# Optimization experiments

Hardware: AMD Instinct MI355X
Metric: run time of the kernel (lower is better)

The kernel has to match this reference:

```python
import jax, jax.numpy as jnp
import numpy as np

N_HEAD = 16
HEAD_DIM = 64
N_EMBD = N_HEAD * HEAD_DIM  # 1024
B, T = 2, 2048


def _rope(x, cos, sin):
    # x: [B,T,H,D]; cos/sin: [1,T,1,D//2]
    d = x.shape[-1] // 2
    x1, x2 = x[..., :d], x[..., d:]
    y1 = x1 * cos + x2 * sin
    y2 = -x1 * sin + x2 * cos
    return jnp.concatenate([y1, y2], axis=-1).astype(x.dtype)


def _rms_norm(x):
    eps = jnp.finfo(x.dtype).eps
    ms = jnp.mean(jnp.square(x), axis=-1, keepdims=True)
    return x * jax.lax.rsqrt(ms + eps)


def setup_inputs() -> dict:
    key = jax.random.key(0)
    ks = jax.random.split(key, 7)
    s = 1.0 / np.sqrt(N_EMBD)
    return {
        "x": jax.random.normal(ks[0], (B, T, N_EMBD), dtype=jnp.float32),
        "cos": jax.random.uniform(ks[1], (1, T, 1, HEAD_DIM // 2), dtype=jnp.float32),
        "sin": jax.random.uniform(ks[2], (1, T, 1, HEAD_DIM // 2), dtype=jnp.float32),
        "Wq": jax.random.normal(ks[3], (N_EMBD, N_EMBD), dtype=jnp.float32) * s,
        "Wk": jax.random.normal(ks[4], (N_EMBD, N_EMBD), dtype=jnp.float32) * s,
        "Wv": jax.random.normal(ks[5], (N_EMBD, N_EMBD), dtype=jnp.float32) * s,
        "Wo": jax.random.normal(ks[6], (N_EMBD, N_EMBD), dtype=jnp.float32) * s,
    }


def reference(x, cos, sin, Wq, Wk, Wv, Wo):
    Bx, Tx, C = x.shape
    # bias-free linear projections (nn.Linear applies x @ W.T)
    q = (x @ Wq.T).reshape(Bx, Tx, N_HEAD, HEAD_DIM)
    k = (x @ Wk.T).reshape(Bx, Tx, N_HEAD, HEAD_DIM)
    v = (x @ Wv.T).reshape(Bx, Tx, N_HEAD, HEAD_DIM)
    # rotary embedding (T == cos length branch)
    q = _rope(q, cos, sin)
    k = _rope(k, cos, sin)
    # QK RMSNorm (no learned scale)
    q = _rms_norm(q)
    k = _rms_norm(k)
    # non-causal SDPA, scale = 1/sqrt(head_dim)
    scale = 1.0 / np.sqrt(HEAD_DIM)
    scores = jnp.einsum("bthd,bshd->bhts", q, k) * scale
    p = jax.nn.softmax(scores, axis=-1)
    y = jnp.einsum("bhts,bshd->bthd", p, v)
    y = y.reshape(Bx, Tx, C)
    return y @ Wo.T
```

## Files before the change

kernel.cpp:

```cpp
#include <hip/hip_runtime.h>
#include <stdint.h>

typedef __attribute__((ext_vector_type(8))) short short8;
typedef __attribute__((ext_vector_type(4))) float floatx4;

#define B_SZ 2
#define T_SZ 2048
#define NH   16
#define HD   64
#define C_SZ 1024
#define M_SZ (B_SZ * T_SZ)

static __device__ __forceinline__ unsigned int cvt2(float a, float b) {
    unsigned int r;
    asm("v_cvt_pk_bf16_f32 %0, %1, %2" : "=v"(r) : "v"(a), "v"(b));
    return r;
}
static __device__ __forceinline__ unsigned short f2bf(float a) {
    return (unsigned short)(cvt2(a, 0.0f) & 0xffffu);
}

static __device__ __forceinline__ void gload_lds16(const void* g, void* l) {
    __builtin_amdgcn_global_load_lds(
        (const __attribute__((address_space(1))) void*)g,
        (__attribute__((address_space(3))) void*)l, 16, 0, 0);
}

__global__ __launch_bounds__(256)
void cvtk(const float* __restrict__ x,
          const float* __restrict__ w0, const float* __restrict__ w1,
          const float* __restrict__ w2, const float* __restrict__ w3,
          unsigned short* __restrict__ xb, unsigned short* __restrict__ wb)
{
    const float* src; unsigned short* dst; int n4;
    const int y = blockIdx.y;
    if (y == 0) { src = x; dst = xb; n4 = (M_SZ * C_SZ) / 4; }
    else {
        src = (y == 1 ? w0 : y == 2 ? w1 : y == 3 ? w2 : w3);
        dst = wb + (size_t)(y - 1) * C_SZ * C_SZ;
        n4 = (C_SZ * C_SZ) / 4;
    }
    for (int i = blockIdx.x * 256 + threadIdx.x; i < n4; i += gridDim.x * 256) {
        float4 f = *(const float4*)&src[(size_t)i * 4];
        uint2 u;
        u.x = cvt2(f.x, f.y);
        u.y = cvt2(f.z, f.w);
        *(uint2*)&dst[(size_t)i * 4] = u;
    }
}

template <int MODE>
__global__ __launch_bounds__(256)
void gemm_nt(const unsigned short* __restrict__ A,
             const unsigned short* __restrict__ Wb,
             const float* __restrict__ cosp,
             const float* __restrict__ sinp,
             unsigned short* __restrict__ qh,
             unsigned short* __restrict__ kh,
             unsigned short* __restrict__ vt,
             float* __restrict__ Cf)
{
    constexpr int K = C_SZ;
    __shared__ __align__(16) unsigned short As[128 * 32];
    __shared__ __align__(16) unsigned short Bs[128 * 32];

    const int tid  = threadIdx.x;
    const int wave = tid >> 6, lane = tid & 63;
    const int wm = wave >> 1, wn = wave & 1;
    const int quad = lane >> 4, l16 = lane & 15;
    const int mb = blockIdx.x * 128, nb = blockIdx.y * 128;
    const int z  = blockIdx.z;

    const unsigned short* Wp = (MODE == 0) ? (Wb + (size_t)z * C_SZ * C_SZ) : Wb;

    floatx4 acc[4][4] = {};

    const int lrow = lane >> 2;
    const int lsw  = lane & 3;

    for (int k0 = 0; k0 < K; k0 += 32) {
        __syncthreads();
        #pragma unroll
        for (int c = 0; c < 2; ++c) {
            int r = (wave * 2 + c) * 16 + lrow;
            int col = ((lsw ^ ((r >> 1) & 3))) * 8;
            gload_lds16(&A[(size_t)(mb + r) * K + k0 + col], &As[(wave * 2 + c) * 512]);
            gload_lds16(&Wp[(size_t)(nb + r) * K + k0 + col], &Bs[(wave * 2 + c) * 512]);
        }
        __syncthreads();

        short8 af[4], bfr[4];
        #pragma unroll
        for (int mt = 0; mt < 4; ++mt) {
            int r = wm * 64 + mt * 16 + l16;
            af[mt] = *(const short8*)&As[r * 32 + ((quad ^ ((r >> 1) & 3)) * 8)];
        }
        #pragma unroll
        for (int nt = 0; nt < 4; ++nt) {
            int r = wn * 64 + nt * 16 + l16;
            bfr[nt] = *(const short8*)&Bs[r * 32 + ((quad ^ ((r >> 1) & 3)) * 8)];
        }
        #pragma unroll
        for (int mt = 0; mt < 4; ++mt)
            #pragma unroll
            for (int nt = 0; nt < 4; ++nt)
                acc[mt][nt] = __builtin_amdgcn_mfma_f32_16x16x32_bf16(
                    af[mt], bfr[nt], acc[mt][nt], 0, 0, 0);
    }

    if (MODE == 1) {
        #pragma unroll
        for (int mt = 0; mt < 4; ++mt)
            #pragma unroll
            for (int nt = 0; nt < 4; ++nt)
                #pragma unroll
                for (int i = 0; i < 4; ++i) {
                    int row = mb + wm * 64 + mt * 16 + quad * 4 + i;
                    int col = nb + wn * 64 + nt * 16 + l16;
                    Cf[(size_t)row * C_SZ + col] = acc[mt][nt][i];
                }
        return;
    }

    const int h = blockIdx.y * 2 + wn;

    if (z == 2) {
        #pragma unroll
        for (int mt = 0; mt < 4; ++mt) {
            int gr0 = mb + wm * 64 + mt * 16 + quad * 4;
            int b = gr0 >> 11, t0 = gr0 & (T_SZ - 1);
            #pragma unroll
            for (int nt = 0; nt < 4; ++nt) {
                int d = nt * 16 + l16;
                uint2 pk;
                pk.x = cvt2(acc[mt][nt][0], acc[mt][nt][1]);
                pk.y = cvt2(acc[mt][nt][2], acc[mt][nt][3]);
                *(uint2*)&vt[((size_t)(b * NH + h) * HD + d) * T_SZ + t0] = pk;
            }
        }
        return;
    }

    unsigned short* dst = (z == 0) ? qh : kh;
    const float qscale = (z == 0) ? (0.125f * 1.4426950408889634f) : 1.0f;
    const float eps = 1.1920929e-07f;

    #pragma unroll
    for (int mt = 0; mt < 4; ++mt) {
        #pragma unroll
        for (int i = 0; i < 4; ++i) {
            int gr = mb + wm * 64 + mt * 16 + quad * 4 + i;
            int b = gr >> 11, t = gr & (T_SZ - 1);
            float ce = cosp[t * 32 + l16];
            float se = sinp[t * 32 + l16];
            float co = cosp[t * 32 + 16 + l16];
            float so = sinp[t * 32 + 16 + l16];
            float a0 = acc[mt][0][i], a1 = acc[mt][1][i];
            float a2 = acc[mt][2][i], a3 = acc[mt][3][i];
            float y0 = a0 * ce + a2 * se;
            float y1 = a1 * co + a3 * so;
            float y2 = a2 * ce - a0 * se;
            float y3 = a3 * co - a1 * so;
            float ss = y0 * y0 + y1 * y1 + y2 * y2 + y3 * y3;
            ss += __shfl_xor(ss, 1, 64);
            ss += __shfl_xor(ss, 2, 64);
            ss += __shfl_xor(ss, 4, 64);
            ss += __shfl_xor(ss, 8, 64);
            float rn = rsqrtf(ss * (1.0f / 64.0f) + eps) * qscale;
            size_t base = ((size_t)(b * NH + h) * T_SZ + t) * (size_t)HD;
            dst[base +  0 + l16] = f2bf(y0 * rn);
            dst[base + 16 + l16] = f2bf(y1 * rn);
            dst[base + 32 + l16] = f2bf(y2 * rn);
            dst[base + 48 + l16] = f2bf(y3 * rn);
        }
    }
}

__global__ __launch_bounds__(512, 4)
void attn(const unsigned short* __restrict__ qh,
          const unsigned short* __restrict__ kh,
          const unsigned short* __restrict__ vt,
          unsigned short* __restrict__ yb)
{
    __shared__ __align__(16) char smem[36864];
    __shared__ float lred[2][128];

    unsigned short* Ks = (unsigned short*)smem;
    unsigned short* Vs = Ks + 64 * 72;
    unsigned short* Psall = Vs + 64 * 72;
    float* Ored = (float*)smem;

    const int tid = threadIdx.x;
    const int wave = tid >> 6, lane = tid & 63;
    const int wk = wave & 1, wq = wave >> 1;
    const int quad = lane >> 4, l16 = lane & 15;
    const int qb = blockIdx.x * 128;
    const int h = blockIdx.y, b = blockIdx.z;

    unsigned short* Ps = Psall + wave * (32 * 36);

    const unsigned short* Qg = qh + ((size_t)(b * NH + h) * T_SZ + qb) * HD;
    const unsigned short* Kg = kh + (size_t)(b * NH + h) * T_SZ * HD;
    const unsigned short* Vg = vt + (size_t)(b * NH + h) * HD * T_SZ;

    short8 qfr[2][2];
    #pragma unroll
    for (int n = 0; n < 2; ++n)
        #pragma unroll
        for (int c = 0; c < 2; ++c)
            qfr[n][c] = *(const short8*)&Qg[(size_t)(wq * 32 + n * 16 + l16) * HD + c * 32 + quad * 8];

    floatx4 o[4][2] = {};
    float l_acc[2] = {0.f, 0.f};

    const int srow = tid >> 3;
    const int scol = (tid & 7) * 8;

    for (int st = 0; st < T_SZ; st += 64) {
        short8 kv = *(const short8*)&Kg[(size_t)(st + srow) * HD + scol];
        short8 vv = *(const short8*)&Vg[(size_t)srow * T_SZ + st + scol];
        *(short8*)&Ks[srow * 72 + scol] = kv;
        *(short8*)&Vs[srow * 72 + scol] = vv;
        __syncthreads();

        floatx4 s[2][2];
        #pragma unroll
        for (int kt = 0; kt < 2; ++kt) {
            const int kr = (wk * 32 + kt * 16 + l16) * 72;
            short8 af0 = *(const short8*)&Ks[kr + quad * 8];
            short8 af1 = *(const short8*)&Ks[kr + 32 + quad * 8];
            #pragma unroll
            for (int n = 0; n < 2; ++n) {
                floatx4 zz = {0.f, 0.f, 0.f, 0.f};
                zz = __builtin_amdgcn_mfma_f32_16x16x32_bf16(af0, qfr[n][0], zz, 0, 0, 0);
                s[kt][n] = __builtin_amdgcn_mfma_f32_16x16x32_bf16(af1, qfr[n][1], zz, 0, 0, 0);
            }
        }

        #pragma unroll
        for (int kt = 0; kt < 2; ++kt)
            #pragma unroll
            for (int n = 0; n < 2; ++n) {
                float p0 = exp2f(s[kt][n][0]);
                float p1 = exp2f(s[kt][n][1]);
                float p2 = exp2f(s[kt][n][2]);
                float p3 = exp2f(s[kt][n][3]);
                l_acc[n] += (p0 + p1) + (p2 + p3);
                uint2 pk;
                pk.x = cvt2(p0, p1);
                pk.y = cvt2(p2, p3);
                *(uint2*)&Ps[(n * 16 + l16) * 36 + kt * 16 + quad * 4] = pk;
            }

        short8 av[4];
        #pragma unroll
        for (int nd = 0; nd < 4; ++nd)
            av[nd] = *(const short8*)&Vs[(nd * 16 + l16) * 72 + wk * 32 + quad * 8];
        #pragma unroll
        for (int nv = 0; nv < 2; ++nv) {
            union { short8 v; uint2 d[2]; } pf;
            pf.d[0] = *(const uint2*)&Ps[(nv * 16 + l16) * 36 + quad * 8];
            pf.d[1] = *(const uint2*)&Ps[(nv * 16 + l16) * 36 + quad * 8 + 4];
            #pragma unroll
            for (int nd = 0; nd < 4; ++nd)
                o[nd][nv] = __builtin_amdgcn_mfma_f32_16x16x32_bf16(av[nd], pf.v, o[nd][nv], 0, 0, 0);
        }
        __syncthreads();
    }

    #pragma unroll
    for (int n = 0; n < 2; ++n) {
        l_acc[n] += __shfl_xor(l_acc[n], 16, 64);
        l_acc[n] += __shfl_xor(l_acc[n], 32, 64);
    }
    if (quad == 0) {
        #pragma unroll
        for (int n = 0; n < 2; ++n)
            lred[wk][wq * 32 + n * 16 + l16] = l_acc[n];
    }
    if (wk == 1) {
        #pragma unroll
        for (int nv = 0; nv < 2; ++nv)
            #pragma unroll
            for (int nd = 0; nd < 4; ++nd)
                *(floatx4*)&Ored[(size_t)wq * (32 * 68) + (nv * 16 + l16) * 68 + nd * 16 + quad * 4] = o[nd][nv];
    }
    __syncthreads();

    if (wk == 0) {
        #pragma unroll
        for (int nv = 0; nv < 2; ++nv) {
            int qi = wq * 32 + nv * 16 + l16;
            float lt = lred[0][qi] + lred[1][qi];
            float inv = 1.0f / lt;
            int t = qb + qi;
            #pragma unroll
            for (int nd = 0; nd < 4; ++nd) {
                floatx4 r = *(const floatx4*)&Ored[(size_t)wq * (32 * 68) + (nv * 16 + l16) * 68 + nd * 16 + quad * 4];
                floatx4 ov = o[nd][nv];
                uint2 u;
                u.x = cvt2((ov[0] + r[0]) * inv, (ov[1] + r[1]) * inv);
                u.y = cvt2((ov[2] + r[2]) * inv, (ov[3] + r[3]) * inv);
                *(uint2*)&yb[((size_t)b * T_SZ + t) * C_SZ + h * 64 + nd * 16 + quad * 4] = u;
            }
        }
    }
}

extern "C" void kernel_launch(void* const* d_in, const int* in_sizes, int n_in,
                              void* d_out, int out_size, void* d_ws, size_t ws_size,
                              hipStream_t stream)
{
    const float* x    = (const float*)d_in[0];
    const float* cosp = (const float*)d_in[1];
    const float* sinp = (const float*)d_in[2];
    const float* Wq   = (const float*)d_in[3];
    const float* Wk   = (const float*)d_in[4];
    const float* Wv   = (const float*)d_in[5];
    const float* Wo   = (const float*)d_in[6];
    float* out = (float*)d_out;

    char* ws = (char*)d_ws;
    unsigned short* xb = (unsigned short*)(ws);
    unsigned short* yb = xb;
    unsigned short* wb = (unsigned short*)(ws + (8u  << 20));
    unsigned short* qh = (unsigned short*)(ws + (16u << 20));
    unsigned short* kh = (unsigned short*)(ws + (24u << 20));
    unsigned short* vt = (unsigned short*)(ws + (32u << 20));

    cvtk<<<dim3(512, 5), 256, 0, stream>>>(x, Wq, Wk, Wv, Wo, xb, wb);
    gemm_nt<0><<<dim3(32, 8, 3), 256, 0, stream>>>(
        xb, wb, cosp, sinp, qh, kh, vt, nullptr);
    attn<<<dim3(16, NH, B_SZ), 512, 0, stream>>>(qh, kh, vt, yb);
    gemm_nt<1><<<dim3(32, 8, 1), 256, 0, stream>>>(
        yb, wb + (size_t)3 * C_SZ * C_SZ, nullptr, nullptr,
        nullptr, nullptr, nullptr, out);
}
```

Measured before the change: 216.3 us.

## Load attention K/V fragments directly from global and double GEMM k-tile

The attention kernel no longer stages K and V tiles through shared memory. Each wave reads its MFMA operand fragments directly from global memory, which removes both block-wide barriers per key tile. The projection GEMM moves to a 64-wide k-step with an 8-way XOR swizzle, halving the loop iterations and barrier count. The cost is redundant global/L2 traffic for K/V across waves and more LDS per GEMM block.

```diff
diff --git a/kernel.cpp b/kernel.cpp
--- a/kernel.cpp
+++ b/kernel.cpp
@@ -61,8 +61,8 @@
              float* __restrict__ Cf)
 {
     constexpr int K = C_SZ;
-    __shared__ __align__(16) unsigned short As[128 * 32];
-    __shared__ __align__(16) unsigned short Bs[128 * 32];
+    __shared__ __align__(16) unsigned short As[128 * 64];
+    __shared__ __align__(16) unsigned short Bs[128 * 64];
 
     const int tid  = threadIdx.x;
     const int wave = tid >> 6, lane = tid & 63;
@@ -75,37 +75,41 @@
 
     floatx4 acc[4][4] = {};
 
-    const int lrow = lane >> 2;
-    const int lsw  = lane & 3;
-
-    for (int k0 = 0; k0 < K; k0 += 32) {
+    const int lrow = lane >> 3;
+    const int lsw  = lane & 7;
+
+    for (int k0 = 0; k0 < K; k0 += 64) {
         __syncthreads();
         #pragma unroll
-        for (int c = 0; c < 2; ++c) {
-            int r = (wave * 2 + c) * 16 + lrow;
-            int col = ((lsw ^ ((r >> 1) & 3))) * 8;
-            gload_lds16(&A[(size_t)(mb + r) * K + k0 + col], &As[(wave * 2 + c) * 512]);
-            gload_lds16(&Wp[(size_t)(nb + r) * K + k0 + col], &Bs[(wave * 2 + c) * 512]);
+        for (int j = 0; j < 4; ++j) {
+            int rb = j * 32 + wave * 8;
+            int r  = rb + lrow;
+            int col = (lsw ^ (r & 7)) * 8;
+            gload_lds16(&A[(size_t)(mb + r) * K + k0 + col], &As[rb * 64]);
+            gload_lds16(&Wp[(size_t)(nb + r) * K + k0 + col], &Bs[rb * 64]);
         }
         __syncthreads();
 
-        short8 af[4], bfr[4];
-        #pragma unroll
-        for (int mt = 0; mt < 4; ++mt) {
-            int r = wm * 64 + mt * 16 + l16;
-            af[mt] = *(const short8*)&As[r * 32 + ((quad ^ ((r >> 1) & 3)) * 8)];
-        }
-        #pragma unroll
-        for (int nt = 0; nt < 4; ++nt) {
-            int r = wn * 64 + nt * 16 + l16;
-            bfr[nt] = *(const short8*)&Bs[r * 32 + ((quad ^ ((r >> 1) & 3)) * 8)];
-        }
-        #pragma unroll
-        for (int mt = 0; mt < 4; ++mt)
-            #pragma unroll
-            for (int nt = 0; nt < 4; ++nt)
-                acc[mt][nt] = __builtin_amdgcn_mfma_f32_16x16x32_bf16(
-                    af[mt], bfr[nt], acc[mt][nt], 0, 0, 0);
+        #pragma unroll
+        for (int kk = 0; kk < 2; ++kk) {
+            short8 af[4], bfr[4];
+            #pragma unroll
+            for (int mt = 0; mt < 4; ++mt) {
+                int r = wm * 64 + mt * 16 + l16;
+                af[mt] = *(const short8*)&As[r * 64 + (((kk * 4 + quad) ^ (r & 7)) * 8)];
+            }
+            #pragma unroll
+            for (int nt = 0; nt < 4; ++nt) {
+                int r = wn * 64 + nt * 16 + l16;
+                bfr[nt] = *(const short8*)&Bs[r * 64 + (((kk * 4 + quad) ^ (r & 7)) * 8)];
+            }
+            #pragma unroll
+            for (int mt = 0; mt < 4; ++mt)
+                #pragma unroll
+                for (int nt = 0; nt < 4; ++nt)
+                    acc[mt][nt] = __builtin_amdgcn_mfma_f32_16x16x32_bf16(
+                        af[mt], bfr[nt], acc[mt][nt], 0, 0, 0);
+        }
     }
 
     if (MODE == 1) {
@@ -182,13 +186,7 @@
           const unsigned short* __restrict__ vt,
           unsigned short* __restrict__ yb)
 {
-    __shared__ __align__(16) char smem[36864];
-    __shared__ float lred[2][128];
-
-    unsigned short* Ks = (unsigned short*)smem;
-    unsigned short* Vs = Ks + 64 * 72;
-    unsigned short* Psall = Vs + 64 * 72;
-    float* Ored = (float*)smem;
+    __shared__ __align__(16) char smem[36864 + 1024];
 
     const int tid = threadIdx.x;
     const int wave = tid >> 6, lane = tid & 63;
@@ -197,7 +195,9 @@
     const int qb = blockIdx.x * 128;
     const int h = blockIdx.y, b = blockIdx.z;
 
-    unsigned short* Ps = Psall + wave * (32 * 36);
+    unsigned short* Ps = (unsigned short*)smem + wave * (32 * 36);
+    float* Ored = (float*)smem;
+    float* lred = (float*)(smem + 36864);
 
     const unsigned short* Qg = qh + ((size_t)(b * NH + h) * T_SZ + qb) * HD;
     const unsigned short* Kg = kh + (size_t)(b * NH + h) * T_SZ * HD;
@@ -210,31 +210,33 @@
         for (int c = 0; c < 2; ++c)
             qfr[n][c] = *(const short8*)&Qg[(size_t)(wq * 32 + n * 16 + l16) * HD + c * 32 + quad * 8];
 
+    const unsigned short* Kp = Kg + (size_t)(wk * 32 + l16) * HD + quad * 8;
+    const unsigned short* Vp = Vg + (size_t)l16 * T_SZ + wk * 32 + quad * 8;
+
     floatx4 o[4][2] = {};
     float l_acc[2] = {0.f, 0.f};
 
-    const int srow = tid >> 3;
-    const int scol = (tid & 7) * 8;
-
     for (int st = 0; st < T_SZ; st += 64) {
-        short8 kv = *(const short8*)&Kg[(size_t)(st + srow) * HD + scol];
-        short8 vv = *(const short8*)&Vg[(size_t)srow * T_SZ + st + scol];
-        *(short8*)&Ks[srow * 72 + scol] = kv;
-        *(short8*)&Vs[srow * 72 + scol] = vv;
-        __syncthreads();
+        short8 a00 = *(const short8*)&Kp[0];
+        short8 a01 = *(const short8*)&Kp[32];
+        short8 a10 = *(const short8*)&Kp[16 * HD];
+        short8 a11 = *(const short8*)&Kp[16 * HD + 32];
+        short8 av0 = *(const short8*)&Vp[0];
+        short8 av1 = *(const short8*)&Vp[16 * T_SZ];
+        short8 av2 = *(const short8*)&Vp[32 * T_SZ];
+        short8 av3 = *(const short8*)&Vp[48 * T_SZ];
+        Kp += 64 * HD;
+        Vp += 64;
 
         floatx4 s[2][2];
         #pragma unroll
-        for (int kt = 0; kt < 2; ++kt) {
-            const int kr = (wk * 32 + kt * 16 + l16) * 72;
-            short8 af0 = *(const short8*)&Ks[kr + quad * 8];
-            short8 af1 = *(const short8*)&Ks[kr + 32 + quad * 8];
-            #pragma unroll
-            for (int n = 0; n < 2; ++n) {
-                floatx4 zz = {0.f, 0.f, 0.f, 0.f};
-                zz = __builtin_amdgcn_mfma_f32_16x16x32_bf16(af0, qfr[n][0], zz, 0, 0, 0);
-                s[kt][n] = __builtin_amdgcn_mfma_f32_16x16x32_bf16(af1, qfr[n][1], zz, 0, 0, 0);
-            }
+        for (int n = 0; n < 2; ++n) {
+            floatx4 z0 = {0.f, 0.f, 0.f, 0.f};
+            z0 = __builtin_amdgcn_mfma_f32_16x16x32_bf16(a00, qfr[n][0], z0, 0, 0, 0);
+            s[0][n] = __builtin_amdgcn_mfma_f32_16x16x32_bf16(a01, qfr[n][1], z0, 0, 0, 0);
+            floatx4 z1 = {0.f, 0.f, 0.f, 0.f};
+            z1 = __builtin_amdgcn_mfma_f32_16x16x32_bf16(a10, qfr[n][0], z1, 0, 0, 0);
+            s[1][n] = __builtin_amdgcn_mfma_f32_16x16x32_bf16(a11, qfr[n][1], z1, 0, 0, 0);
         }
 
         #pragma unroll
@@ -252,20 +254,16 @@
                 *(uint2*)&Ps[(n * 16 + l16) * 36 + kt * 16 + quad * 4] = pk;
             }
 
-        short8 av[4];
-        #pragma unroll
-        for (int nd = 0; nd < 4; ++nd)
-            av[nd] = *(const short8*)&Vs[(nd * 16 + l16) * 72 + wk * 32 + quad * 8];
         #pragma unroll
         for (int nv = 0; nv < 2; ++nv) {
             union { short8 v; uint2 d[2]; } pf;
             pf.d[0] = *(const uint2*)&Ps[(nv * 16 + l16) * 36 + quad * 8];
             pf.d[1] = *(const uint2*)&Ps[(nv * 16 + l16) * 36 + quad * 8 + 4];
-            #pragma unroll
-            for (int nd = 0; nd < 4; ++nd)
-                o[nd][nv] = __builtin_amdgcn_mfma_f32_16x16x32_bf16(av[nd], pf.v, o[nd][nv], 0, 0, 0);
-        }
-        __syncthreads();
+            o[0][nv] = __builtin_amdgcn_mfma_f32_16x16x32_bf16(av0, pf.v, o[0][nv], 0, 0, 0);
+            o[1][nv] = __builtin_amdgcn_mfma_f32_16x16x32_bf16(av1, pf.v, o[1][nv], 0, 0, 0);
+            o[2][nv] = __builtin_amdgcn_mfma_f32_16x16x32_bf16(av2, pf.v, o[2][nv], 0, 0, 0);
+            o[3][nv] = __builtin_amdgcn_mfma_f32_16x16x32_bf16(av3, pf.v, o[3][nv], 0, 0, 0);
+        }
     }
 
     #pragma unroll
@@ -276,8 +274,10 @@
     if (quad == 0) {
         #pragma unroll
         for (int n = 0; n < 2; ++n)
-            lred[wk][wq * 32 + n * 16 + l16] = l_acc[n];
-    }
+            lred[wk * 128 + wq * 32 + n * 16 + l16] = l_acc[n];
+    }
+    __syncthreads();
+
     if (wk == 1) {
         #pragma unroll
         for (int nv = 0; nv < 2; ++nv)
@@ -291,7 +291,7 @@
         #pragma unroll
         for (int nv = 0; nv < 2; ++nv) {
             int qi = wq * 32 + nv * 16 + l16;
-            float lt = lred[0][qi] + lred[1][qi];
+            float lt = lred[qi] + lred[128 + qi];
             float inv = 1.0f / lt;
             int t = qb + qi;
             #pragma unroll
```

New measurement: 267.0 us. 1.23x slower.
